# Kernel optimization log

Hardware: AMD Instinct MI355X
Metric: run time of the kernel (lower is better)

## Reference

```python
import jax, jax.numpy as jnp
import numpy as np

B, S, D, H = 16, 512, 512, 8
DH = D // H
EPS = 1e-5
NEG = -1.0e9


def _layernorm(v, g, b):
    mu = jnp.mean(v, axis=-1, keepdims=True)
    var = jnp.mean(jnp.square(v - mu), axis=-1, keepdims=True)
    return (v - mu) * jax.lax.rsqrt(var + EPS) * g + b


def setup_inputs() -> dict:
    key = jax.random.key(0)
    ks = jax.random.split(key, 12)
    sd = 1.0 / np.sqrt(D)
    return {
        "x": jax.random.normal(ks[0], (B, S, D), dtype=jnp.float32),
        "mask": jax.random.randint(ks[1], (B, S, S), 0, 2, dtype=jnp.int32),
        "ln_g": jnp.ones((D,), jnp.float32),
        "ln_b": jnp.zeros((D,), jnp.float32),
        "lna_g": jnp.ones((S,), jnp.float32),  # LayerNorm over attention scores (last dim = S = model_dim)
        "lna_b": jnp.zeros((S,), jnp.float32),
        "Wq": jax.random.uniform(ks[2], (D, D), jnp.float32, -sd, sd),
        "bq": jnp.zeros((D,), jnp.float32),
        "Wk": jax.random.uniform(ks[3], (D, D), jnp.float32, -sd, sd),
        "bk": jnp.zeros((D,), jnp.float32),
        "Wv": jax.random.uniform(ks[4], (D, D), jnp.float32, -sd, sd),
        "bv": jnp.zeros((D,), jnp.float32),
        "Wd": jax.random.uniform(ks[5], (D, D), jnp.float32, -sd, sd),
        "bd": jnp.zeros((D,), jnp.float32),
    }


def reference(x, mask, ln_g, ln_b, lna_g, lna_b, Wq, bq, Wk, bk, Wv, bv, Wd, bd):
    # pre-LN
    h = _layernorm(x, ln_g, ln_b)  # [B,S,D]
    # projections -> [B,H,S,DH]
    q = (h @ Wq + bq).reshape(B, S, H, DH).transpose(0, 2, 1, 3)
    k = (h @ Wk + bk).reshape(B, S, H, DH).transpose(0, 2, 1, 3)
    v = (h @ Wv + bv).reshape(B, S, H, DH).transpose(0, 2, 1, 3)
    # raw scores [B,H,S,S]
    scores = jnp.einsum("bhqd,bhkd->bhqk", q, k) / jnp.sqrt(jnp.asarray(DH, x.dtype))
    # non-standard: LayerNorm over the key axis of the score matrix
    scores = _layernorm(scores, lna_g, lna_b)
    # mask (broadcast over heads), then softmax
    scores = jnp.where(mask[:, None, :, :] == 0, jnp.asarray(NEG, x.dtype), scores)
    attn = jax.nn.softmax(scores, axis=-1)
    # dropout omitted (eval mode / deterministic reference)
    out = jnp.einsum("bhqk,bhkd->bhqd", attn, v)
    out = out.transpose(0, 2, 1, 3).reshape(B, S, D)
    out = out @ Wd + bd
    return out + x
```

## Files before the change

kernel.cpp:

```cpp
#include <hip/hip_runtime.h>
#include <hip/hip_bf16.h>
#include <stdint.h>


typedef __hip_bfloat16 bf16;
typedef __bf16 bf16x8 __attribute__((ext_vector_type(8)));
typedef float f32x4 __attribute__((ext_vector_type(4)));

#define MFMA16(a, b, c) __builtin_amdgcn_mfma_f32_16x16x32_bf16((a), (b), (c), 0, 0, 0)

static __device__ __forceinline__ bf16 f2b(float v) { return __float2bfloat16(v); }
static __device__ __forceinline__ bf16x8 ld8(const bf16* p) { return *(const bf16x8*)p; }
static __device__ __forceinline__ uint16_t f2bu(float v) {
  return __hip_bfloat16_raw(__float2bfloat16(v)).x;
}
static __device__ __forceinline__ float bu2f(uint32_t u) {
  union { uint32_t i; float f; } c;
  c.i = u << 16;
  return c.f;
}
static __device__ __forceinline__ void stage16(const bf16* g, bf16* l) {
  __builtin_amdgcn_global_load_lds(
      (const __attribute__((address_space(1))) void*)g,
      (__attribute__((address_space(3))) void*)l, 16, 0, 0);
}

__global__ __launch_bounds__(256) void prep(
    const float* __restrict__ x, const float* __restrict__ lng,
    const float* __restrict__ lnb, bf16* __restrict__ h,
    const int* __restrict__ mask, uint32_t* __restrict__ bits,
    const float* __restrict__ W0, const float* __restrict__ W1,
    const float* __restrict__ W2, const float* __restrict__ W3,
    bf16* __restrict__ T0, bf16* __restrict__ T1,
    bf16* __restrict__ T2, bf16* __restrict__ T3) {
  __shared__ float t[32][33];
  const int bid = blockIdx.x;
  const int tid = threadIdx.x;
  const int w = tid >> 6, lane = tid & 63;

  if (bid < 2048) {
    int row = bid * 4 + w;
    const float* xr = x + (size_t)row * 512 + lane * 8;
    float4 v0 = *(const float4*)xr;
    float4 v1 = *(const float4*)(xr + 4);
    float s  = v0.x + v0.y + v0.z + v0.w + v1.x + v1.y + v1.z + v1.w;
    float s2 = v0.x * v0.x + v0.y * v0.y + v0.z * v0.z + v0.w * v0.w +
               v1.x * v1.x + v1.y * v1.y + v1.z * v1.z + v1.w * v1.w;
#pragma unroll
    for (int m = 1; m < 64; m <<= 1) {
      s += __shfl_xor(s, m);
      s2 += __shfl_xor(s2, m);
    }
    float mean = s * (1.0f / 512.0f);
    float var = s2 * (1.0f / 512.0f) - mean * mean;
    float rstd = rsqrtf(var + 1e-5f);
    const float4 g0 = *(const float4*)(lng + lane * 8);
    const float4 g1 = *(const float4*)(lng + lane * 8 + 4);
    const float4 b0 = *(const float4*)(lnb + lane * 8);
    const float4 b1 = *(const float4*)(lnb + lane * 8 + 4);
    union { uint16_t u[8]; bf16x8 v; } o;
    o.u[0] = f2bu((v0.x - mean) * rstd * g0.x + b0.x);
    o.u[1] = f2bu((v0.y - mean) * rstd * g0.y + b0.y);
    o.u[2] = f2bu((v0.z - mean) * rstd * g0.z + b0.z);
    o.u[3] = f2bu((v0.w - mean) * rstd * g0.w + b0.w);
    o.u[4] = f2bu((v1.x - mean) * rstd * g1.x + b1.x);
    o.u[5] = f2bu((v1.y - mean) * rstd * g1.y + b1.y);
    o.u[6] = f2bu((v1.z - mean) * rstd * g1.z + b1.z);
    o.u[7] = f2bu((v1.w - mean) * rstd * g1.w + b1.w);
    *(bf16x8*)(h + (size_t)row * 512 + lane * 8) = o.v;
  } else if (bid < 6144) {
    size_t base = (size_t)(bid - 2048) * 1024 + w * 64 + lane;
#pragma unroll
    for (int it = 0; it < 4; it++) {
      size_t e = base + it * 256;
      int mv = mask[e];
      unsigned long long bal = __ballot(mv != 0);
      if (lane == 0) ((unsigned long long*)bits)[e >> 6] = bal;
    }
  } else {
    int tt = bid - 6144;
    int wsel = tt >> 8, rem = tt & 255;
    int n0 = (rem & 15) * 32, k0 = (rem >> 4) * 32;
    const float* src; bf16* dst;
    switch (wsel) {
      case 0: src = W0; dst = T0; break;
      case 1: src = W1; dst = T1; break;
      case 2: src = W2; dst = T2; break;
      default: src = W3; dst = T3; break;
    }
    int tx = tid & 31, ty = tid >> 5;
#pragma unroll
    for (int i = 0; i < 4; i++) {
      int kk = ty * 4 + i;
      t[kk][tx] = src[(k0 + kk) * 512 + n0 + tx];
    }
    __syncthreads();
#pragma unroll
    for (int i = 0; i < 4; i++) {
      int nn = ty * 4 + i;
      dst[(n0 + nn) * 512 + k0 + tx] = f2b(t[tx][nn]);
    }
  }
}

__global__ __launch_bounds__(256) void gemm_qkv(
    const bf16* __restrict__ hm,
    const bf16* __restrict__ WT0, const bf16* __restrict__ WT1, const bf16* __restrict__ WT2,
    const float* __restrict__ bq, const float* __restrict__ bk, const float* __restrict__ bv,
    bf16* __restrict__ outq, bf16* __restrict__ outk, bf16* __restrict__ outvT) {
  const int sel = blockIdx.z;
  const bf16* WT = sel == 0 ? WT0 : (sel == 1 ? WT1 : WT2);
  const float* bias = sel == 0 ? bq : (sel == 1 ? bk : bv);
  __shared__ __align__(16) uint16_t SM[128 * 136];
  bf16* As = (bf16*)SM;
  bf16* Bs = (bf16*)(SM + 4096);
  int tid = threadIdx.x;
  int w = tid >> 6, lane = tid & 63, q4 = lane >> 4, l16 = lane & 15;
  int wr = w >> 1, wc = w & 1;
  int m0 = blockIdx.x * 128, n0 = blockIdx.y * 128;
  f32x4 acc[4][4];
#pragma unroll
  for (int i = 0; i < 4; i++)
#pragma unroll
    for (int j = 0; j < 4; j++) acc[i][j] = (f32x4){0.f, 0.f, 0.f, 0.f};

  for (int kc = 0; kc < 16; kc++) {
    int k0 = kc * 32;
#pragma unroll
    for (int u0 = 0; u0 < 2; u0++) {
      int e = u0 * 256 + tid;
      int row = e >> 2, c8 = (e & 3) * 8;
      stage16(&hm[(size_t)(m0 + row) * 512 + k0 + c8], &As[e * 8]);
      stage16(&WT[(size_t)(n0 + row) * 512 + k0 + c8], &Bs[e * 8]);
    }
    __syncthreads();
    bf16x8 af[4], bfr[4];
#pragma unroll
    for (int rt = 0; rt < 4; rt++)
      af[rt] = ld8(&As[(wr * 64 + rt * 16 + l16) * 32 + q4 * 8]);
#pragma unroll
    for (int nt = 0; nt < 4; nt++)
      bfr[nt] = ld8(&Bs[(wc * 64 + nt * 16 + l16) * 32 + q4 * 8]);
#pragma unroll
    for (int rt = 0; rt < 4; rt++)
#pragma unroll
      for (int nt = 0; nt < 4; nt++) acc[rt][nt] = MFMA16(af[rt], bfr[nt], acc[rt][nt]);
    __syncthreads();
  }

  if (sel != 2) {
    const float scale = sel == 0 ? 0.125f : 1.0f;
#pragma unroll
    for (int rt = 0; rt < 4; rt++)
#pragma unroll
      for (int nt = 0; nt < 4; nt++) {
        int ncol = wc * 64 + nt * 16 + l16;
        float bsv = bias[n0 + ncol];
#pragma unroll
        for (int r = 0; r < 4; r++) {
          int mrow = wr * 64 + rt * 16 + q4 * 4 + r;
          SM[mrow * 136 + ncol] = f2bu((acc[rt][nt][r] + bsv) * scale);
        }
      }
    __syncthreads();
    bf16* dst = sel == 0 ? outq : outk;
#pragma unroll
    for (int p = 0; p < 8; p++) {
      int e = p * 256 + tid;
      int row = e >> 4, c8 = (e & 15) * 8;
      bf16x8 vv = *(bf16x8*)&SM[row * 136 + c8];
      int gm = m0 + row, b_ = gm >> 9, s_ = gm & 511;
      int n = n0 + c8, hh = n >> 6, dh = n & 63;
      *(bf16x8*)(dst + ((size_t)((b_ * 8 + hh) * 512 + s_)) * 64 + dh) = vv;
    }
  } else {
#pragma unroll
    for (int rt = 0; rt < 4; rt++)
#pragma unroll
      for (int nt = 0; nt < 4; nt++) {
        int ncol = wc * 64 + nt * 16 + l16;
        float bsv = bias[n0 + ncol];
        union { uint16_t q[4]; uint2 u; } pk;
#pragma unroll
        for (int r = 0; r < 4; r++) pk.q[r] = f2bu(acc[rt][nt][r] + bsv);
        *(uint2*)&SM[ncol * 136 + wr * 64 + rt * 16 + q4 * 4] = pk.u;
      }
    __syncthreads();
#pragma unroll
    for (int p = 0; p < 8; p++) {
      int e = p * 256 + tid;
      int nn = e >> 4, s8 = (e & 15) * 8;
      bf16x8 vv = *(bf16x8*)&SM[nn * 136 + s8];
      int n = n0 + nn, hh = n >> 6, dh = n & 63;
      int gm = m0 + s8, b_ = gm >> 9, s_ = gm & 511;
      *(bf16x8*)(outvT + ((size_t)((b_ * 8 + hh) * 64 + dh)) * 512 + s_) = vv;
    }
  }
}

__global__ __launch_bounds__(256, 4) void attn_fused(
    const bf16* __restrict__ q, const bf16* __restrict__ k, const bf16* __restrict__ vT,
    const uint32_t* __restrict__ bits, const float* __restrict__ lg,
    const float* __restrict__ lb, bf16* __restrict__ ctx) {
  const int id = blockIdx.x;
  const int xcd = id & 7;
  const int j = id >> 3;
  const int mt = j & 7;
  const int bh = ((j >> 3) << 3) | xcd;
  const int m0 = mt * 64;
  const int b = bh >> 3, hh = bh & 7;
  const int tid = threadIdx.x;
  const int w = tid >> 6, lane = tid & 63, q4 = lane >> 4, l16 = lane & 15;

  __shared__ __align__(16) bf16 SBk[2][32 * 72];
  __shared__ __align__(16) bf16 SBv[2][64 * 40];
  __shared__ uint32_t GB[512];
  __shared__ uint32_t sbits[64][17];

  GB[tid] = (uint32_t)f2bu(lg[tid]) | ((uint32_t)f2bu(lb[tid]) << 16);
  GB[tid + 256] = (uint32_t)f2bu(lg[tid + 256]) | ((uint32_t)f2bu(lb[tid + 256]) << 16);
  {
    int row = tid >> 2, g = tid & 3;
    const uint32_t* src = bits + ((size_t)b * 512 + m0 + row) * 16 + g * 4;
    uint4 u = *(const uint4*)src;
    sbits[row][g * 4] = u.x; sbits[row][g * 4 + 1] = u.y;
    sbits[row][g * 4 + 2] = u.z; sbits[row][g * 4 + 3] = u.w;
  }

  const bf16* qb = q + ((size_t)bh * 512 + m0 + w * 16) * 64;
  const bf16* kb = k + (size_t)bh * 512 * 64;
  const bf16* vb = vT + (size_t)bh * 64 * 512;

  bf16x8 aq0 = ld8(qb + (size_t)l16 * 64 + q4 * 8);
  bf16x8 aq1 = ld8(qb + (size_t)l16 * 64 + 32 + q4 * 8);

  const int key0 = tid >> 3, dh8 = (tid & 7) * 8;
  const int dhv = tid >> 2, kk8 = (tid & 3) * 8;

  *(bf16x8*)&SBk[0][key0 * 72 + dh8] = ld8(kb + (size_t)key0 * 64 + dh8);
  __syncthreads();

  float s = 0.f, s2 = 0.f;
  for (int c = 0; c < 16; c++) {
    const int buf = c & 1;
    bf16x8 rk;
    if (c < 15) rk = ld8(kb + (size_t)((c + 1) * 32 + key0) * 64 + dh8);
    __builtin_amdgcn_s_setprio(1);
#pragma unroll
    for (int kg = 0; kg < 2; kg++) {
      const bf16* kp = &SBk[buf][(kg * 16 + l16) * 72];
      bf16x8 b0 = ld8(kp + q4 * 8);
      bf16x8 b1 = ld8(kp + 32 + q4 * 8);
      f32x4 acc = (f32x4){0.f, 0.f, 0.f, 0.f};
      acc = MFMA16(b0, aq0, acc);
      acc = MFMA16(b1, aq1, acc);
#pragma unroll
      for (int r = 0; r < 4; r++) {
        float v = acc[r];
        s += v;
        s2 += v * v;
      }
    }
    __builtin_amdgcn_s_setprio(0);
    if (c < 15)
      *(bf16x8*)&SBk[buf ^ 1][key0 * 72 + dh8] = rk;
    __syncthreads();
  }
  s += __shfl_xor(s, 16);  s += __shfl_xor(s, 32);
  s2 += __shfl_xor(s2, 16); s2 += __shfl_xor(s2, 32);
  const float mean = s * (1.0f / 512.0f);
  const float rstd = rsqrtf(s2 * (1.0f / 512.0f) - mean * mean + 1e-5f);

  *(bf16x8*)&SBk[0][key0 * 72 + dh8] = ld8(kb + (size_t)key0 * 64 + dh8);
  *(bf16x8*)&SBv[0][dhv * 40 + kk8] = ld8(vb + (size_t)dhv * 512 + kk8);
  __syncthreads();

  f32x4 o[4];
#pragma unroll
  for (int nt = 0; nt < 4; nt++) o[nt] = (f32x4){0.f, 0.f, 0.f, 0.f};
  float se = 0.f;
  const int src0 = ((q4 & 1) * 2) * 16 + l16;
  const int src1 = src0 + 16;
  const bool hi = (q4 >> 1) != 0;

  for (int c = 0; c < 16; c++) {
    const int buf = c & 1;
    bf16x8 rk, rv;
    if (c < 15) {
      rk = ld8(kb + (size_t)((c + 1) * 32 + key0) * 64 + dh8);
      rv = ld8(vb + (size_t)dhv * 512 + (c + 1) * 32 + kk8);
    }
    const uint32_t dw = sbits[w * 16 + l16][c];
    uint32_t Pk[2][2];
#pragma unroll
    for (int kg = 0; kg < 2; kg++) {
      const bf16* kp = &SBk[buf][(kg * 16 + l16) * 72];
      bf16x8 b0 = ld8(kp + q4 * 8);
      bf16x8 b1 = ld8(kp + 32 + q4 * 8);
      f32x4 acc = (f32x4){0.f, 0.f, 0.f, 0.f};
      __builtin_amdgcn_s_setprio(1);
      acc = MFMA16(b0, aq0, acc);
      acc = MFMA16(b1, aq1, acc);
      __builtin_amdgcn_s_setprio(0);
      uint4 gb4 = *(uint4*)&GB[c * 32 + kg * 16 + q4 * 4];
      uint16_t p[4];
#pragma unroll
      for (int r = 0; r < 4; r++) {
        uint32_t gb = r == 0 ? gb4.x : (r == 1 ? gb4.y : (r == 2 ? gb4.z : gb4.w));
        float t = (acc[r] - mean) * rstd * bu2f(gb & 0xffffu) + bu2f(gb >> 16);
        t = ((dw >> (kg * 16 + q4 * 4 + r)) & 1u) ? t : -1.0e9f;
        float pf = __expf(t);
        se += pf;
        p[r] = f2bu(pf);
      }
      Pk[kg][0] = (uint32_t)p[0] | ((uint32_t)p[1] << 16);
      Pk[kg][1] = (uint32_t)p[2] | ((uint32_t)p[3] << 16);
    }
    uint32_t t00 = __shfl(Pk[0][0], src0), t01 = __shfl(Pk[1][0], src0);
    uint32_t t10 = __shfl(Pk[0][1], src0), t11 = __shfl(Pk[1][1], src0);
    uint32_t t20 = __shfl(Pk[0][0], src1), t21 = __shfl(Pk[1][0], src1);
    uint32_t t30 = __shfl(Pk[0][1], src1), t31 = __shfl(Pk[1][1], src1);
    union { uint32_t d[4]; bf16x8 v; } af;
    af.d[0] = hi ? t01 : t00;
    af.d[1] = hi ? t11 : t10;
    af.d[2] = hi ? t21 : t20;
    af.d[3] = hi ? t31 : t30;
    __builtin_amdgcn_s_setprio(1);
#pragma unroll
    for (int nt = 0; nt < 4; nt++) {
      bf16x8 bv8 = ld8(&SBv[buf][(nt * 16 + l16) * 40 + q4 * 8]);
      o[nt] = MFMA16(af.v, bv8, o[nt]);
    }
    __builtin_amdgcn_s_setprio(0);
    if (c < 15) {
      *(bf16x8*)&SBk[buf ^ 1][key0 * 72 + dh8] = rk;
      *(bf16x8*)&SBv[buf ^ 1][dhv * 40 + kk8] = rv;
    }
    __syncthreads();
  }

  se += __shfl_xor(se, 16);
  se += __shfl_xor(se, 32);
  float invr = 1.0f / se;
  float inv[4];
#pragma unroll
  for (int r = 0; r < 4; r++) inv[r] = __shfl(invr, q4 * 4 + r);

  bf16* cb = ctx + ((size_t)b * 512 + m0 + w * 16) * 512 + hh * 64;
#pragma unroll
  for (int nt = 0; nt < 4; nt++)
#pragma unroll
    for (int r = 0; r < 4; r++)
      cb[(size_t)(q4 * 4 + r) * 512 + nt * 16 + l16] = f2b(o[nt][r] * inv[r]);
}

__global__ __launch_bounds__(256) void gemm_out(
    const bf16* __restrict__ ctx, const bf16* __restrict__ WT,
    const float* __restrict__ bd, const float* __restrict__ x, float* __restrict__ out) {
  __shared__ __align__(16) bf16 As[64 * 32];
  __shared__ __align__(16) bf16 Bs[128 * 32];
  int tid = threadIdx.x;
  int w = tid >> 6, lane = tid & 63, q4 = lane >> 4, l16 = lane & 15;
  int m0 = blockIdx.x * 64, n0 = blockIdx.y * 128;
  f32x4 acc[4][2];
#pragma unroll
  for (int i = 0; i < 4; i++)
#pragma unroll
    for (int j = 0; j < 2; j++) acc[i][j] = (f32x4){0.f, 0.f, 0.f, 0.f};

  for (int kc = 0; kc < 16; kc++) {
    int k0 = kc * 32;
    {
      int e = tid;
      int row = e >> 2, c8 = (e & 3) * 8;
      stage16(&ctx[(size_t)(m0 + row) * 512 + k0 + c8], &As[e * 8]);
    }
#pragma unroll
    for (int u0 = 0; u0 < 2; u0++) {
      int e = u0 * 256 + tid;
      int row = e >> 2, c8 = (e & 3) * 8;
      stage16(&WT[(size_t)(n0 + row) * 512 + k0 + c8], &Bs[e * 8]);
    }
    __syncthreads();
    bf16x8 af[4], bfr[2];
#pragma unroll
    for (int rt = 0; rt < 4; rt++)
      af[rt] = ld8(&As[(rt * 16 + l16) * 32 + q4 * 8]);
#pragma unroll
    for (int nt = 0; nt < 2; nt++)
      bfr[nt] = ld8(&Bs[(w * 32 + nt * 16 + l16) * 32 + q4 * 8]);
#pragma unroll
    for (int rt = 0; rt < 4; rt++)
#pragma unroll
      for (int nt = 0; nt < 2; nt++) acc[rt][nt] = MFMA16(af[rt], bfr[nt], acc[rt][nt]);
    __syncthreads();
  }
#pragma unroll
  for (int rt = 0; rt < 4; rt++) {
    int mbase = m0 + rt * 16 + q4 * 4;
#pragma unroll
    for (int nt = 0; nt < 2; nt++) {
      int n = n0 + w * 32 + nt * 16 + l16;
      float bsv = bd[n];
#pragma unroll
      for (int r = 0; r < 4; r++) {
        size_t idx = (size_t)(mbase + r) * 512 + n;
        out[idx] = acc[rt][nt][r] + bsv + x[idx];
      }
    }
  }
}

extern "C" void kernel_launch(void* const* d_in, const int* in_sizes, int n_in,
                              void* d_out, int out_size, void* d_ws, size_t ws_size,
                              hipStream_t stream) {
  const float* x = (const float*)d_in[0];
  const int* mask = (const int*)d_in[1];
  const float* ln_g = (const float*)d_in[2];
  const float* ln_b = (const float*)d_in[3];
  const float* lna_g = (const float*)d_in[4];
  const float* lna_b = (const float*)d_in[5];
  const float* Wq = (const float*)d_in[6];
  const float* bq = (const float*)d_in[7];
  const float* Wk = (const float*)d_in[8];
  const float* bk = (const float*)d_in[9];
  const float* Wv = (const float*)d_in[10];
  const float* bv = (const float*)d_in[11];
  const float* Wd = (const float*)d_in[12];
  const float* bd = (const float*)d_in[13];

  char* ws = (char*)d_ws;
  const size_t MB = 1024 * 1024;
  if (ws_size < 44 * MB) return;
  bf16* h = (bf16*)(ws);
  bf16* qd = (bf16*)(ws + 8 * MB);
  bf16* kd = (bf16*)(ws + 16 * MB);
  bf16* vTd = (bf16*)(ws + 24 * MB);
  bf16* ctx = (bf16*)(ws + 32 * MB);
  bf16* WqT = (bf16*)(ws + 40 * MB);
  bf16* WkT = (bf16*)(ws + 40 * MB + 512 * 1024);
  bf16* WvT = (bf16*)(ws + 40 * MB + 1024 * 1024);
  bf16* WdT = (bf16*)(ws + 40 * MB + 1536 * 1024);
  uint32_t* bits = (uint32_t*)(ws + 42 * MB);

  prep<<<7168, 256, 0, stream>>>(x, ln_g, ln_b, h, mask, bits,
                                 Wq, Wk, Wv, Wd, WqT, WkT, WvT, WdT);
  gemm_qkv<<<dim3(64, 4, 3), 256, 0, stream>>>(h, WqT, WkT, WvT, bq, bk, bv, qd, kd, vTd);
  attn_fused<<<1024, 256, 0, stream>>>(qd, kd, vTd, bits, lna_g, lna_b, ctx);
  gemm_out<<<dim3(128, 4), 256, 0, stream>>>(ctx, WdT, bd, x, (float*)d_out);
}
```

Before: 171.6 us.

## Double-buffer LDS staging in QKV projection GEMM with async prefetch

The QKV GEMM now prefetches the next K-slice of activations and weights into a second LDS buffer via direct global-to-LDS loads. It then waits only for the previous slice with a partial vmcnt wait, so global load latency overlaps with the MFMA work. The shared array already had room for two buffers. The cost is hand-managed waitcnt and barrier logic, which must stay correct for the LDS-DMA ordering. This GEMM is only one of several kernels in the pipeline.

```diff
diff --git a/kernel.cpp b/kernel.cpp
--- a/kernel.cpp
+++ b/kernel.cpp
@@ -112,8 +112,7 @@
   const bf16* WT = sel == 0 ? WT0 : (sel == 1 ? WT1 : WT2);
   const float* bias = sel == 0 ? bq : (sel == 1 ? bk : bv);
   __shared__ __align__(16) uint16_t SM[128 * 136];
-  bf16* As = (bf16*)SM;
-  bf16* Bs = (bf16*)(SM + 4096);
+  bf16* buf = (bf16*)SM;
   int tid = threadIdx.x;
   int w = tid >> 6, lane = tid & 63, q4 = lane >> 4, l16 = lane & 15;
   int wr = w >> 1, wc = w & 1;
@@ -124,28 +123,52 @@
 #pragma unroll
     for (int j = 0; j < 4; j++) acc[i][j] = (f32x4){0.f, 0.f, 0.f, 0.f};
 
+  const int srow = tid >> 2, sc8 = (tid & 3) * 8;
+  const int srow1 = (256 + tid) >> 2, sc81 = ((256 + tid) & 3) * 8;
+
+  {
+    bf16* As = buf;
+    bf16* Bs = buf + 4096;
+    stage16(&hm[(size_t)(m0 + srow) * 512 + sc8], &As[(size_t)tid * 8]);
+    stage16(&WT[(size_t)(n0 + srow) * 512 + sc8], &Bs[(size_t)tid * 8]);
+    stage16(&hm[(size_t)(m0 + srow1) * 512 + sc81], &As[(size_t)(256 + tid) * 8]);
+    stage16(&WT[(size_t)(n0 + srow1) * 512 + sc81], &Bs[(size_t)(256 + tid) * 8]);
+  }
+
+  int cur = 0;
   for (int kc = 0; kc < 16; kc++) {
-    int k0 = kc * 32;
-#pragma unroll
-    for (int u0 = 0; u0 < 2; u0++) {
-      int e = u0 * 256 + tid;
-      int row = e >> 2, c8 = (e & 3) * 8;
-      stage16(&hm[(size_t)(m0 + row) * 512 + k0 + c8], &As[e * 8]);
-      stage16(&WT[(size_t)(n0 + row) * 512 + k0 + c8], &Bs[e * 8]);
-    }
-    __syncthreads();
-    bf16x8 af[4], bfr[4];
-#pragma unroll
-    for (int rt = 0; rt < 4; rt++)
-      af[rt] = ld8(&As[(wr * 64 + rt * 16 + l16) * 32 + q4 * 8]);
-#pragma unroll
-    for (int nt = 0; nt < 4; nt++)
-      bfr[nt] = ld8(&Bs[(wc * 64 + nt * 16 + l16) * 32 + q4 * 8]);
-#pragma unroll
-    for (int rt = 0; rt < 4; rt++)
-#pragma unroll
-      for (int nt = 0; nt < 4; nt++) acc[rt][nt] = MFMA16(af[rt], bfr[nt], acc[rt][nt]);
-    __syncthreads();
+    if (kc < 15) {
+      int k0 = (kc + 1) * 32;
+      bf16* As = buf + (cur ^ 1) * 8192;
+      bf16* Bs = As + 4096;
+      stage16(&hm[(size_t)(m0 + srow) * 512 + k0 + sc8], &As[(size_t)tid * 8]);
+      stage16(&WT[(size_t)(n0 + srow) * 512 + k0 + sc8], &Bs[(size_t)tid * 8]);
+      stage16(&hm[(size_t)(m0 + srow1) * 512 + k0 + sc81], &As[(size_t)(256 + tid) * 8]);
+      stage16(&WT[(size_t)(n0 + srow1) * 512 + k0 + sc81], &Bs[(size_t)(256 + tid) * 8]);
+      asm volatile("s_waitcnt vmcnt(4)" ::: "memory");
+    } else {
+      asm volatile("s_waitcnt vmcnt(0)" ::: "memory");
+    }
+    __builtin_amdgcn_s_barrier();
+    __builtin_amdgcn_sched_barrier(0);
+    {
+      bf16* As = buf + cur * 8192;
+      bf16* Bs = As + 4096;
+      bf16x8 af[4], bfr[4];
+#pragma unroll
+      for (int rt = 0; rt < 4; rt++)
+        af[rt] = ld8(&As[(wr * 64 + rt * 16 + l16) * 32 + q4 * 8]);
+#pragma unroll
+      for (int nt = 0; nt < 4; nt++)
+        bfr[nt] = ld8(&Bs[(wc * 64 + nt * 16 + l16) * 32 + q4 * 8]);
+#pragma unroll
+      for (int rt = 0; rt < 4; rt++)
+#pragma unroll
+        for (int nt = 0; nt < 4; nt++) acc[rt][nt] = MFMA16(af[rt], bfr[nt], acc[rt][nt]);
+    }
+    __builtin_amdgcn_sched_barrier(0);
+    __builtin_amdgcn_s_barrier();
+    cur ^= 1;
   }
 
   if (sel != 2) {
```

Result: no change. 170.5 us (-0.7%).
